# Performance work log

Hardware: AMD Instinct MI355X
Metric: run time of the kernel (lower is better)

Reference implementation:

```python
import jax, jax.numpy as jnp
import numpy as np

EPS = 1e-6
NEG_SLOPE = 0.2


def knn_idx(xf, k):
    # xf: (B, C, N) flattened vector features; returns (B, N, k) neighbor indices
    xx = jnp.sum(xf * xf, axis=1)                       # (B, N)
    inner = jnp.einsum('bcn,bcm->bnm', xf, xf)          # (B, N, N)
    neg_dist = 2.0 * inner - xx[:, :, None] - xx[:, None, :]  # -||xi-xj||^2
    _, idx = jax.lax.top_k(neg_dist, k)                 # includes self (dist 0)
    return idx


def get_graph_feature(x, k):
    # x: (B, D, 3, N) -> edge features (B, 2D, 3, N, k)
    B, D, _, N = x.shape
    idx = knn_idx(x.reshape(B, D * 3, N), k)            # (B, N, k)
    pts = jnp.transpose(x, (0, 3, 1, 2))                # (B, N, D, 3)
    neigh = jax.vmap(lambda p, i: p[i])(pts, idx)       # (B, N, k, D, 3) gather
    center = jnp.broadcast_to(pts[:, :, None], neigh.shape)
    feat = jnp.concatenate([neigh - center, center], axis=3)  # (B, N, k, 2D, 3)
    return jnp.transpose(feat, (0, 3, 4, 1, 2))


def vn_linear_leakyrelu(x, Wf, Wd):
    # Vector-Neuron linear + leaky ReLU. x: (B, Cin, 3, ...),
    # Wf: (Cout, Cin), Wd: (Cout, Cin) or (1, Cin) when nonlinearity is shared.
    p = jnp.einsum('oi,bi...->bo...', Wf, x)
    d = jnp.einsum('oi,bi...->bo...', Wd, x)
    dot = jnp.sum(p * d, axis=2, keepdims=True)
    dsq = jnp.sum(d * d, axis=2, keepdims=True)
    proj = p - (dot / (dsq + EPS)) * d
    return NEG_SLOPE * p + (1.0 - NEG_SLOPE) * jnp.where(dot >= 0, p, proj)


def setup_inputs() -> dict:
    key = jax.random.key(0)
    ks = jax.random.split(key, 11)
    B, N = 8, 1024
    x = jax.random.normal(ks[0], (B, 3, N), dtype=jnp.float32)
    # dims = [1, 21, 21, 42, 85, 341]
    ins = [2, 42, 42, 84, 169]      # 2*dim_in for edge layers; sum(dims[1:-1]) for last
    outs = [21, 21, 42, 85, 341]
    dirs = [21, 21, 42, 85, 1]      # last layer has share_nonlinearity=True
    d = {"x": x}
    for i, (ci, co, cd) in enumerate(zip(ins, outs, dirs)):
        s = 1.0 / np.sqrt(ci)
        kf, kd = jax.random.split(ks[1 + i])
        d[f"Wf{i}"] = (jax.random.normal(kf, (co, ci), dtype=jnp.float32) * s)
        d[f"Wd{i}"] = (jax.random.normal(kd, (cd, ci), dtype=jnp.float32) * s)
    d["k"] = 20
    return d


def reference(x, Wf0, Wd0, Wf1, Wd1, Wf2, Wd2, Wf3, Wd3, Wf4, Wd4, k):
    cur = x[:, None]                 # (B, 1, 3, N)
    feats = []
    for Wf, Wd in ((Wf0, Wd0), (Wf1, Wd1), (Wf2, Wd2), (Wf3, Wd3)):
        g = get_graph_feature(cur, k)        # (B, 2D, 3, N, k)
        h = vn_linear_leakyrelu(g, Wf, Wd)   # (B, Dout, 3, N, k)
        cur = h.mean(axis=-1)                # mean over neighbors -> (B, Dout, 3, N)
        feats.append(cur)
    xcat = jnp.concatenate(feats, axis=1)    # (B, 169, 3, N)
    out = vn_linear_leakyrelu(xcat, Wf4, Wd4)
    return out.mean(axis=-1)                 # mean over points -> (B, 341, 3)
```

## Files before the change

### kernel.cpp

```cpp
#include <hip/hip_runtime.h>
#include <cstddef>

#define BB 8
#define NN 1024
#define KK 20
#define CCAT 169
#define NT 16

__global__ __launch_bounds__(256) void dist_tile_kernel(
    const float* __restrict__ src, int bs, int F, float* __restrict__ dist) {
  __shared__ float As[8][128];
  __shared__ float Bs[8][128];
  int b = blockIdx.z;
  int rem = blockIdx.x, bi = 0;
  while (rem >= 8 - bi) { rem -= 8 - bi; ++bi; }
  int bj = bi + rem;
  int n0 = bi * 128;
  int m0 = bj * 128;
  int t = threadIdx.x;
  int tx = t & 15, ty = t >> 4;
  const float* p = src + (size_t)b * bs;

  float acc[8][8];
  float xn[8], xm[8];
#pragma unroll
  for (int i = 0; i < 8; ++i) {
    xn[i] = 0.f;
    xm[i] = 0.f;
#pragma unroll
    for (int j = 0; j < 8; ++j) acc[i][j] = 0.f;
  }

  int fr = t >> 5;
  int cc = (t & 31) << 2;
  for (int f0 = 0; f0 < F; f0 += 8) {
    int f = f0 + fr;
    float4 av = {0.f, 0.f, 0.f, 0.f}, bv = {0.f, 0.f, 0.f, 0.f};
    if (f < F) {
      av = *(const float4*)(p + (size_t)f * NN + n0 + cc);
      bv = *(const float4*)(p + (size_t)f * NN + m0 + cc);
    }
    __syncthreads();
    *(float4*)&As[fr][cc] = av;
    *(float4*)&Bs[fr][cc] = bv;
    __syncthreads();
#pragma unroll
    for (int f2 = 0; f2 < 8; ++f2) {
      float4 al = *(const float4*)&As[f2][ty << 2];
      float4 ah = *(const float4*)&As[f2][64 + (ty << 2)];
      float4 bl = *(const float4*)&Bs[f2][tx << 2];
      float4 bh = *(const float4*)&Bs[f2][64 + (tx << 2)];
      float a[8] = {al.x, al.y, al.z, al.w, ah.x, ah.y, ah.z, ah.w};
      float bb[8] = {bl.x, bl.y, bl.z, bl.w, bh.x, bh.y, bh.z, bh.w};
#pragma unroll
      for (int i = 0; i < 8; ++i) xn[i] += a[i] * a[i];
#pragma unroll
      for (int j = 0; j < 8; ++j) xm[j] += bb[j] * bb[j];
#pragma unroll
      for (int i = 0; i < 8; ++i)
#pragma unroll
        for (int j = 0; j < 8; ++j) acc[i][j] += a[i] * bb[j];
    }
  }

#pragma unroll
  for (int i = 0; i < 8; ++i)
#pragma unroll
    for (int j = 0; j < 8; ++j) acc[i][j] = 2.f * acc[i][j] - xn[i] - xm[j];

#pragma unroll
  for (int i = 0; i < 8; ++i) {
    int n = n0 + ((i < 4) ? ((ty << 2) + i) : (64 + (ty << 2) + i - 4));
    float* dr = dist + (((size_t)b * NN + n) << 10);
    *(float4*)(dr + m0 + (tx << 2)) =
        make_float4(acc[i][0], acc[i][1], acc[i][2], acc[i][3]);
    *(float4*)(dr + m0 + 64 + (tx << 2)) =
        make_float4(acc[i][4], acc[i][5], acc[i][6], acc[i][7]);
  }

  if (bi != bj) {
#pragma unroll
    for (int j = 0; j < 8; ++j) {
      int m = m0 + ((j < 4) ? ((tx << 2) + j) : (64 + (tx << 2) + j - 4));
      float* dr = dist + (((size_t)b * NN + m) << 10);
      *(float4*)(dr + n0 + (ty << 2)) =
          make_float4(acc[0][j], acc[1][j], acc[2][j], acc[3][j]);
      *(float4*)(dr + n0 + 64 + (ty << 2)) =
          make_float4(acc[4][j], acc[5][j], acc[6][j], acc[7][j]);
    }
  }
}

__device__ __forceinline__ unsigned long long shfl_xor_u64(
    unsigned long long v, int off) {
  unsigned lo = (unsigned)v, hi = (unsigned)(v >> 32);
  lo = __shfl_xor(lo, off, 64);
  hi = __shfl_xor(hi, off, 64);
  return ((unsigned long long)hi << 32) | lo;
}

__global__ __launch_bounds__(256) void topk_kernel(
    const float* __restrict__ dist, int* __restrict__ idx_out) {
  int wave = threadIdx.x >> 6;
  int lane = threadIdx.x & 63;
  int row = blockIdx.x * 4 + wave;
  const float* d = dist + ((size_t)row << 10);

  unsigned long long key[16];
#pragma unroll
  for (int s = 0; s < 16; ++s) {
    int m = lane + (s << 6);
    unsigned u = __float_as_uint(d[m]);
    u = (u & 0x80000000u) ? ~u : (u | 0x80000000u);
    key[s] = ((unsigned long long)u << 32) | (unsigned)(NN - 1 - m);
  }

#pragma unroll
  for (int size = 2; size <= 16; size <<= 1) {
#pragma unroll
    for (int stride = size >> 1; stride > 0; stride >>= 1) {
#pragma unroll
      for (int i = 0; i < 16; ++i) {
        int j = i ^ stride;
        if (j > i) {
          unsigned long long a = key[i], c = key[j];
          bool desc = ((i & size) == 0);
          bool sw = desc ? (a < c) : (a > c);
          key[i] = sw ? c : a;
          key[j] = sw ? a : c;
        }
      }
    }
  }

  int* out = idx_out + row * KK;
  unsigned long long head = key[0];
  for (int r = 0; r < KK; ++r) {
    unsigned long long w = head;
#pragma unroll
    for (int off = 32; off > 0; off >>= 1) {
      unsigned long long o = shfl_xor_u64(w, off);
      if (o > w) w = o;
    }
    if (lane == 0) out[r] = (NN - 1) - (int)(w & 0xFFFFFFFFull);
    if (head == w) {
#pragma unroll
      for (int s = 0; s < 15; ++s) key[s] = key[s + 1];
      key[15] = 0ull;
      head = key[0];
    }
  }
}

__global__ __launch_bounds__(256) void edge_fused_kernel(
    const float* __restrict__ src, int bs, int D, int Co,
    const float* __restrict__ Wf, const float* __restrict__ Wd,
    const int* __restrict__ idx, int ooff, float* __restrict__ xcat) {
  __shared__ float2 Ulds[3 * NN];
  __shared__ float2 Vlds[3 * NN];
  __shared__ float4 Wlds[48];
  int bo = blockIdx.x;
  int b = bo / Co, o = bo % Co;
  int t = threadIdx.x;

  if (t < D) {
    float wfa = Wf[o * 2 * D + t];
    float wfb = Wf[o * 2 * D + D + t] - wfa;
    float wda = Wd[o * 2 * D + t];
    float wdb = Wd[o * 2 * D + D + t] - wda;
    Wlds[t] = make_float4(wfa, wfb, wda, wdb);
  }
  __syncthreads();

  const float* sb = src + (size_t)b * bs;
#pragma unroll
  for (int r = 0; r < 3; ++r) {
    int g = t + 256 * r;
    float4 uf = {0.f, 0.f, 0.f, 0.f}, vf = {0.f, 0.f, 0.f, 0.f};
    float4 ud = {0.f, 0.f, 0.f, 0.f}, vd = {0.f, 0.f, 0.f, 0.f};
    for (int i = 0; i < D; ++i) {
      float4 s = *(const float4*)(sb + (size_t)i * 3 * NN + (g << 2));
      float4 w = Wlds[i];
      uf.x += w.x * s.x; uf.y += w.x * s.y; uf.z += w.x * s.z; uf.w += w.x * s.w;
      vf.x += w.y * s.x; vf.y += w.y * s.y; vf.z += w.y * s.z; vf.w += w.y * s.w;
      ud.x += w.z * s.x; ud.y += w.z * s.y; ud.z += w.z * s.z; ud.w += w.z * s.w;
      vd.x += w.w * s.x; vd.y += w.w * s.y; vd.z += w.w * s.z; vd.w += w.w * s.w;
    }
    *(float4*)&Ulds[(g << 2) + 0] = make_float4(uf.x, ud.x, uf.y, ud.y);
    *(float4*)&Ulds[(g << 2) + 2] = make_float4(uf.z, ud.z, uf.w, ud.w);
    *(float4*)&Vlds[(g << 2) + 0] = make_float4(vf.x, vd.x, vf.y, vd.y);
    *(float4*)&Vlds[(g << 2) + 2] = make_float4(vf.z, vd.z, vf.w, vd.w);
  }
  __syncthreads();

  const float inv_k = 1.f / KK;
#pragma unroll
  for (int rep = 0; rep < 4; ++rep) {
    int n = rep * 256 + t;
    float2 v0 = Vlds[n];
    float2 v1 = Vlds[NN + n];
    float2 v2 = Vlds[2 * NN + n];
    const int4* ip = (const int4*)(idx + (b * NN + n) * KK);
    float a0 = 0.f, a1 = 0.f, a2 = 0.f;
#pragma unroll
    for (int q = 0; q < 5; ++q) {
      int4 iv = ip[q];
      int nbs[4] = {iv.x, iv.y, iv.z, iv.w};
#pragma unroll
      for (int jj = 0; jj < 4; ++jj) {
        int nb = nbs[jj];
        float2 u0 = Ulds[nb];
        float2 u1 = Ulds[NN + nb];
        float2 u2 = Ulds[2 * NN + nb];
        float pf0 = u0.x + v0.x, pd0 = u0.y + v0.y;
        float pf1 = u1.x + v1.x, pd1 = u1.y + v1.y;
        float pf2 = u2.x + v2.x, pd2 = u2.y + v2.y;
        float dot = pf0 * pd0 + pf1 * pd1 + pf2 * pd2;
        float dsq = pd0 * pd0 + pd1 * pd1 + pd2 * pd2;
        float g = (dot >= 0.f) ? 0.f : 0.8f * dot / (dsq + 1e-6f);
        a0 += pf0 - g * pd0;
        a1 += pf1 - g * pd1;
        a2 += pf2 - g * pd2;
      }
    }
    size_t ob = (size_t)b * CCAT * 3 * NN + (size_t)(ooff + o) * 3 * NN + n;
    xcat[ob] = a0 * inv_k;
    xcat[ob + NN] = a1 * inv_k;
    xcat[ob + 2 * NN] = a2 * inv_k;
  }
}

__global__ __launch_bounds__(256) void final_fused_kernel(
    const float* __restrict__ xcat, const float* __restrict__ Wf4,
    const float* __restrict__ Wd4, float* __restrict__ part) {
  __shared__ float Ws[32][64];
  __shared__ float Xs[3][32][64];
  __shared__ float Wda[192];
  int b = blockIdx.z;
  int o0 = blockIdx.y * 64;
  int n0 = blockIdx.x * 64;
  int t = threadIdx.x;
  int tx = t & 15, ty = t >> 4;

  if (t < 192) Wda[t] = (t < CCAT) ? Wd4[t] : 0.f;

  float acc[3][4][4];
  float dv[3][4];
#pragma unroll
  for (int c = 0; c < 3; ++c) {
#pragma unroll
    for (int i = 0; i < 4; ++i)
#pragma unroll
      for (int j = 0; j < 4; ++j) acc[c][i][j] = 0.f;
#pragma unroll
    for (int j = 0; j < 4; ++j) dv[c][j] = 0.f;
  }

  const float* xb = xcat + (size_t)b * CCAT * 3 * NN;
  const int NTILE = (CCAT + 31) / 32;

  for (int tt = 0; tt < NTILE; ++tt) {
    float4 xv[2][3];
    float wv[2][4];
#pragma unroll
    for (int r = 0; r < 2; ++r) {
      int f = tt * 32 + r * 16 + ty;
#pragma unroll
      for (int c = 0; c < 3; ++c) {
        xv[r][c] = make_float4(0.f, 0.f, 0.f, 0.f);
        if (f < CCAT)
          xv[r][c] =
              *(const float4*)(xb + ((size_t)f * 3 + c) * NN + n0 + (tx << 2));
      }
#pragma unroll
      for (int q = 0; q < 4; ++q) {
        int o = o0 + (tx << 2) + q;
        wv[r][q] = (o < 341 && f < CCAT) ? Wf4[(size_t)o * CCAT + f] : 0.f;
      }
    }
    __syncthreads();
#pragma unroll
    for (int r = 0; r < 2; ++r) {
#pragma unroll
      for (int c = 0; c < 3; ++c)
        *(float4*)&Xs[c][r * 16 + ty][tx << 2] = xv[r][c];
      *(float4*)&Ws[r * 16 + ty][tx << 2] =
          make_float4(wv[r][0], wv[r][1], wv[r][2], wv[r][3]);
    }
    __syncthreads();
#pragma unroll
    for (int f2 = 0; f2 < 32; ++f2) {
      float4 w = *(const float4*)&Ws[f2][ty << 2];
      float wa[4] = {w.x, w.y, w.z, w.w};
      float wd = Wda[tt * 32 + f2];
#pragma unroll
      for (int c = 0; c < 3; ++c) {
        float4 x = *(const float4*)&Xs[c][f2][tx << 2];
        float xa[4] = {x.x, x.y, x.z, x.w};
#pragma unroll
        for (int j = 0; j < 4; ++j) dv[c][j] += wd * xa[j];
#pragma unroll
        for (int i = 0; i < 4; ++i)
#pragma unroll
          for (int j = 0; j < 4; ++j) acc[c][i][j] += wa[i] * xa[j];
      }
    }
  }

  float s[3][4];
#pragma unroll
  for (int c = 0; c < 3; ++c)
#pragma unroll
    for (int i = 0; i < 4; ++i) s[c][i] = 0.f;
#pragma unroll
  for (int i = 0; i < 4; ++i) {
#pragma unroll
    for (int j = 0; j < 4; ++j) {
      float d0 = dv[0][j], d1 = dv[1][j], d2 = dv[2][j];
      float p0 = acc[0][i][j], p1 = acc[1][i][j], p2 = acc[2][i][j];
      float dot = p0 * d0 + p1 * d1 + p2 * d2;
      float dsq = d0 * d0 + d1 * d1 + d2 * d2;
      float g = (dot >= 0.f) ? 0.f : 0.8f * dot / (dsq + 1e-6f);
      s[0][i] += p0 - g * d0;
      s[1][i] += p1 - g * d1;
      s[2][i] += p2 - g * d2;
    }
  }

#pragma unroll
  for (int off = 1; off < 16; off <<= 1) {
#pragma unroll
    for (int c = 0; c < 3; ++c)
#pragma unroll
      for (int i = 0; i < 4; ++i) s[c][i] += __shfl_xor(s[c][i], off, 64);
  }
  if (tx == 0) {
#pragma unroll
    for (int i = 0; i < 4; ++i) {
      int o = o0 + (ty << 2) + i;
      if (o < 341) {
#pragma unroll
        for (int c = 0; c < 3; ++c)
          part[(((size_t)b * 341 + o) * 3 + c) * NT + blockIdx.x] = s[c][i];
      }
    }
  }
}

__global__ void final_reduce_kernel(const float* __restrict__ part,
                                    float* __restrict__ out) {
  int t = blockIdx.x * 256 + threadIdx.x;
  if (t >= BB * 341 * 3) return;
  const float* p = part + (size_t)t * NT;
  float s = 0.f;
#pragma unroll
  for (int nt = 0; nt < NT; ++nt) s += p[nt];
  out[t] = s * (1.f / 1024.f);
}

extern "C" void kernel_launch(void* const* d_in, const int* in_sizes, int n_in,
                              void* d_out, int out_size, void* d_ws,
                              size_t ws_size, hipStream_t stream) {
  (void)in_sizes; (void)n_in; (void)out_size; (void)ws_size;
  const float* x = (const float*)d_in[0];
  const float* Wf[5] = {(const float*)d_in[1], (const float*)d_in[3],
                        (const float*)d_in[5], (const float*)d_in[7],
                        (const float*)d_in[9]};
  const float* Wd[5] = {(const float*)d_in[2], (const float*)d_in[4],
                        (const float*)d_in[6], (const float*)d_in[8],
                        (const float*)d_in[10]};

  float* ws = (float*)d_ws;
  float* dist = ws;
  float* part = ws;
  size_t off = (size_t)BB * NN * NN;
  int* idx = (int*)(ws + off);
  off += (size_t)BB * NN * KK;
  float* xcat = ws + off;

  struct LayerCfg { int D, Co, inoff, ooff; };
  const LayerCfg L[4] = {
      {1, 21, 0, 0},
      {21, 21, 0, 21},
      {21, 42, 21, 42},
      {42, 85, 42, 84},
  };

  for (int l = 0; l < 4; ++l) {
    const float* src = (l == 0) ? x : (xcat + (size_t)L[l].inoff * 3 * NN);
    int bs = (l == 0) ? 3 * NN : CCAT * 3 * NN;
    int D = L[l].D, Co = L[l].Co;

    dist_tile_kernel<<<dim3(36, 1, BB), 256, 0, stream>>>(src, bs, 3 * D, dist);
    topk_kernel<<<(BB * NN) / 4, 256, 0, stream>>>(dist, idx);
    edge_fused_kernel<<<BB * Co, 256, 0, stream>>>(src, bs, D, Co, Wf[l],
                                                   Wd[l], idx, L[l].ooff,
                                                   xcat);
  }

  final_fused_kernel<<<dim3(NT, 6, BB), 256, 0, stream>>>(xcat, Wf[4], Wd[4],
                                                          part);
  final_reduce_kernel<<<(BB * 341 * 3 + 255) / 256, 256, 0, stream>>>(
      part, (float*)d_out);
}
```

Before: 451.4 us.

## Split edge kernel over point ranges and shrink final GEMM K-tile

The edge kernel gets a second grid dimension that splits the per-point gather/aggregation phase across several blocks for the narrow early layers (4, 4, 2, 1 splits). This raises block count and occupancy where few (batch, output) blocks exist, at the cost of each split block recomputing the full U/V projection over all points. Separately, the final fused kernel's K-tile drops from 32 to 16 features, with the Wd vector loaded per tile instead of preloaded. This halves LDS usage to allow more resident blocks, but adds more loop iterations and barriers.

Result: faster. 431.8 us (-4.4%).

```diff
diff --git a/kernel.cpp b/kernel.cpp
--- a/kernel.cpp
+++ b/kernel.cpp
@@ -153,7 +153,7 @@
 }
 
 __global__ __launch_bounds__(256) void edge_fused_kernel(
-    const float* __restrict__ src, int bs, int D, int Co,
+    const float* __restrict__ src, int bs, int D, int Co, int nsplit,
     const float* __restrict__ Wf, const float* __restrict__ Wd,
     const int* __restrict__ idx, int ooff, float* __restrict__ xcat) {
   __shared__ float2 Ulds[3 * NN];
@@ -194,9 +194,9 @@
   __syncthreads();
 
   const float inv_k = 1.f / KK;
-#pragma unroll
-  for (int rep = 0; rep < 4; ++rep) {
-    int n = rep * 256 + t;
+  int cnt = NN / nsplit;
+  int nbase = blockIdx.y * cnt;
+  for (int n = nbase + t; n < nbase + cnt; n += 256) {
     float2 v0 = Vlds[n];
     float2 v1 = Vlds[NN + n];
     float2 v2 = Vlds[2 * NN + n];
@@ -233,17 +233,15 @@
 __global__ __launch_bounds__(256) void final_fused_kernel(
     const float* __restrict__ xcat, const float* __restrict__ Wf4,
     const float* __restrict__ Wd4, float* __restrict__ part) {
-  __shared__ float Ws[32][64];
-  __shared__ float Xs[3][32][64];
-  __shared__ float Wda[192];
+  __shared__ float Ws[16][64];
+  __shared__ float Xs[3][16][64];
+  __shared__ float Wds[16];
   int b = blockIdx.z;
   int o0 = blockIdx.y * 64;
   int n0 = blockIdx.x * 64;
   int t = threadIdx.x;
   int tx = t & 15, ty = t >> 4;
 
-  if (t < 192) Wda[t] = (t < CCAT) ? Wd4[t] : 0.f;
-
   float acc[3][4][4];
   float dv[3][4];
 #pragma unroll
@@ -257,42 +255,34 @@
   }
 
   const float* xb = xcat + (size_t)b * CCAT * 3 * NN;
-  const int NTILE = (CCAT + 31) / 32;
-
-  for (int tt = 0; tt < NTILE; ++tt) {
-    float4 xv[2][3];
-    float wv[2][4];
-#pragma unroll
-    for (int r = 0; r < 2; ++r) {
-      int f = tt * 32 + r * 16 + ty;
-#pragma unroll
-      for (int c = 0; c < 3; ++c) {
-        xv[r][c] = make_float4(0.f, 0.f, 0.f, 0.f);
-        if (f < CCAT)
-          xv[r][c] =
-              *(const float4*)(xb + ((size_t)f * 3 + c) * NN + n0 + (tx << 2));
-      }
-#pragma unroll
-      for (int q = 0; q < 4; ++q) {
-        int o = o0 + (tx << 2) + q;
-        wv[r][q] = (o < 341 && f < CCAT) ? Wf4[(size_t)o * CCAT + f] : 0.f;
-      }
-    }
+  for (int f0 = 0; f0 < CCAT; f0 += 16) {
+    int f = f0 + ty;
+    float4 xv[3];
+#pragma unroll
+    for (int c = 0; c < 3; ++c) {
+      xv[c] = make_float4(0.f, 0.f, 0.f, 0.f);
+      if (f < CCAT)
+        xv[c] = *(const float4*)(xb + ((size_t)f * 3 + c) * NN + n0 + (tx << 2));
+    }
+    float wv[4];
+#pragma unroll
+    for (int q = 0; q < 4; ++q) {
+      int o = o0 + (tx << 2) + q;
+      wv[q] = (o < 341 && f < CCAT) ? Wf4[o * CCAT + f] : 0.f;
+    }
+    float wdv = 0.f;
+    if (t < 16 && f0 + t < CCAT) wdv = Wd4[f0 + t];
     __syncthreads();
 #pragma unroll
-    for (int r = 0; r < 2; ++r) {
-#pragma unroll
-      for (int c = 0; c < 3; ++c)
-        *(float4*)&Xs[c][r * 16 + ty][tx << 2] = xv[r][c];
-      *(float4*)&Ws[r * 16 + ty][tx << 2] =
-          make_float4(wv[r][0], wv[r][1], wv[r][2], wv[r][3]);
-    }
+    for (int c = 0; c < 3; ++c) *(float4*)&Xs[c][ty][tx << 2] = xv[c];
+    *(float4*)&Ws[ty][tx << 2] = make_float4(wv[0], wv[1], wv[2], wv[3]);
+    if (t < 16) Wds[t] = wdv;
     __syncthreads();
 #pragma unroll
-    for (int f2 = 0; f2 < 32; ++f2) {
+    for (int f2 = 0; f2 < 16; ++f2) {
       float4 w = *(const float4*)&Ws[f2][ty << 2];
       float wa[4] = {w.x, w.y, w.z, w.w};
-      float wd = Wda[tt * 32 + f2];
+      float wd = Wds[f2];
 #pragma unroll
       for (int c = 0; c < 3; ++c) {
         float4 x = *(const float4*)&Xs[c][f2][tx << 2];
@@ -378,12 +368,12 @@
   off += (size_t)BB * NN * KK;
   float* xcat = ws + off;
 
-  struct LayerCfg { int D, Co, inoff, ooff; };
+  struct LayerCfg { int D, Co, inoff, ooff, nsplit; };
   const LayerCfg L[4] = {
-      {1, 21, 0, 0},
-      {21, 21, 0, 21},
-      {21, 42, 21, 42},
-      {42, 85, 42, 84},
+      {1, 21, 0, 0, 4},
+      {21, 21, 0, 21, 4},
+      {21, 42, 21, 42, 2},
+      {42, 85, 42, 84, 1},
   };
 
   for (int l = 0; l < 4; ++l) {
@@ -393,9 +383,8 @@
 
     dist_tile_kernel<<<dim3(36, 1, BB), 256, 0, stream>>>(src, bs, 3 * D, dist);
     topk_kernel<<<(BB * NN) / 4, 256, 0, stream>>>(dist, idx);
-    edge_fused_kernel<<<BB * Co, 256, 0, stream>>>(src, bs, D, Co, Wf[l],
-                                                   Wd[l], idx, L[l].ooff,
-                                                   xcat);
+    edge_fused_kernel<<<dim3(BB * Co, L[l].nsplit), 256, 0, stream>>>(
+        src, bs, D, Co, L[l].nsplit, Wf[l], Wd[l], idx, L[l].ooff, xcat);
   }
 
   final_fused_kernel<<<dim3(NT, 6, BB), 256, 0, stream>>>(xcat, Wf[4], Wd[4],
```
